# Performance work log

Hardware: AMD Instinct MI355X
Metric: run time of the kernel (lower is better)

Reference implementation:

```python
import jax, jax.numpy as jnp
import numpy as np

P = 16           # patch size
D = 768          # embed / feature dim (= 3*P*P)
T = 8            # number of task vectors
H_META = 192     # MetaNet hidden (= D // 4)


def patchify(x):
    # x: [B, 3, H, W] -> [B, N, 3*P*P]
    B, C, H, W = x.shape
    x = x.reshape(B, C, H // P, P, W // P, P)
    x = x.transpose(0, 2, 4, 1, 3, 5)
    return x.reshape(B, (H // P) * (W // P), C * P * P)


def encode(W1, b1, W2, b2, x):
    # base functional encoder f(params, x): shared weights over the batch
    patches = patchify(x)                       # [B, N, D]
    h = jax.nn.relu(patches @ W1 + b1)          # [B, N, D]
    pooled = h.mean(axis=1)                     # [B, D]
    return pooled @ W2 + b2                     # [B, D]


def setup_inputs() -> dict:
    key = jax.random.key(0)
    ks = jax.random.split(key, 14)
    B = 64
    s = 0.02
    return {
        "x":   jax.random.normal(ks[0], (B, 3, 224, 224), jnp.float32),
        # base model params
        "W1":  jax.random.normal(ks[1], (D, D), jnp.float32) * s,
        "b1":  jax.random.normal(ks[2], (D,), jnp.float32) * s,
        "W2":  jax.random.normal(ks[3], (D, D), jnp.float32) * s,
        "b2":  jax.random.normal(ks[4], (D,), jnp.float32) * s,
        # task-vector deltas (stacked over T tasks)
        "dW1": jax.random.normal(ks[5], (T, D, D), jnp.float32) * s,
        "db1": jax.random.normal(ks[6], (T, D), jnp.float32) * s,
        "dW2": jax.random.normal(ks[7], (T, D, D), jnp.float32) * s,
        "db2": jax.random.normal(ks[8], (T, D), jnp.float32) * s,
        # MetaNet (Linear-ReLU-Linear); zero-init in the original, random here
        "mw1": jax.random.normal(ks[9], (D, H_META), jnp.float32) * s,
        "mb1": jax.random.normal(ks[10], (H_META,), jnp.float32) * s,
        "mw2": jax.random.normal(ks[11], (H_META, T), jnp.float32) * s,
        "mb2": jax.random.normal(ks[12], (T,), jnp.float32) * s,
    }


def reference(x, W1, b1, W2, b2, dW1, db1, dW2, db2, mw1, mb1, mw2, mb2):
    # 1) base features with frozen base model (torch.no_grad)
    base = jax.lax.stop_gradient(encode(W1, b1, W2, b2, x))       # [B, D]
    # 2) per-sample mixing coefficients via MetaNet
    coefs = jax.nn.relu(base @ mw1 + mb1) @ mw2 + mb2             # [B, T]
    # 3) per-sample mixed parameters: p + sum_t c[b,t] * dp[t]
    nW1 = W1 + jnp.einsum("bt,tij->bij", coefs, dW1)              # [B, D, D]
    nb1 = b1 + coefs @ db1                                        # [B, D]
    nW2 = W2 + jnp.einsum("bt,tij->bij", coefs, dW2)              # [B, D, D]
    nb2 = b2 + coefs @ db2                                        # [B, D]
    # 4) batched per-sample forward with the mixed weights
    patches = patchify(x)                                         # [B, N, D]
    h = jax.nn.relu(jnp.einsum("bnd,bde->bne", patches, nW1) + nb1[:, None, :])
    pooled = h.mean(axis=1)                                       # [B, D]
    out = jnp.einsum("bd,bde->be", pooled, nW2) + nb2             # [B, D]
    return out
```

## Files before the change

kernel.cpp:

```cpp
#include <hip/hip_runtime.h>
#include <hip/hip_bf16.h>


typedef __bf16 bf16x8 __attribute__((ext_vector_type(8)));
typedef float f32x4 __attribute__((ext_vector_type(4)));
typedef __hip_bfloat16 bf16;

struct alignas(16) BF8 { bf16 h[8]; };

constexpr int BATCH = 64;
constexpr int NP    = 196;
constexpr int NPAD  = 256;
constexpr int DIM   = 768;
constexpr int NT    = 8;
constexpr size_t MSZ = (size_t)DIM * DIM;

__device__ __forceinline__ void async_cp16(const void* g, void* l) {
  __builtin_amdgcn_global_load_lds(
      (const __attribute__((address_space(1))) uint32_t*)g,
      (__attribute__((address_space(3))) uint32_t*)l, 16, 0, 0);
}

__global__ void k_patchify(const float* __restrict__ x, bf16* __restrict__ A) {
  int idx  = blockIdx.x * blockDim.x + threadIdx.x;
  int col4 = idx % (DIM / 4);
  int row  = idx / (DIM / 4);
  int d = col4 * 4;
  int b = row >> 8;
  int n = row & 255;
  bf16 tmp[4];
  if (n < NP) {
    int hp = n / 14, wp = n % 14;
    int c  = d >> 8;
    int rr = d & 255;
    int i = rr >> 4, j = rr & 15;
    const float* src = x + ((((size_t)b * 3 + c) * 224 + hp * 16 + i) * 224 + wp * 16 + j);
    float4 f = *(const float4*)src;
    tmp[0] = __float2bfloat16(f.x);
    tmp[1] = __float2bfloat16(f.y);
    tmp[2] = __float2bfloat16(f.z);
    tmp[3] = __float2bfloat16(f.w);
  } else {
    tmp[0] = tmp[1] = tmp[2] = tmp[3] = __float2bfloat16(0.0f);
  }
  *(ushort4*)(A + (size_t)row * DIM + d) = *(ushort4*)tmp;
}

__global__ void k_transpose_cast(const float* __restrict__ W1, const float* __restrict__ dW1,
                                 const float* __restrict__ W2, const float* __restrict__ dW2,
                                 bf16* __restrict__ WT) {
  __shared__ float tile[32][33];
  int mat = blockIdx.z;
  const float* src;
  if      (mat == 0) src = W1;
  else if (mat <= 8) src = dW1 + (size_t)(mat - 1) * MSZ;
  else if (mat == 9) src = W2;
  else               src = dW2 + (size_t)(mat - 10) * MSZ;
  int n0 = blockIdx.x * 32;
  int k0 = blockIdx.y * 32;
  int tx = threadIdx.x & 31, ty = threadIdx.x >> 5;
#pragma unroll
  for (int r = ty; r < 32; r += 8)
    tile[r][tx] = src[(size_t)(k0 + r) * DIM + n0 + tx];
  __syncthreads();
  bf16* dst = WT + (size_t)mat * MSZ;
#pragma unroll
  for (int r = ty; r < 32; r += 8)
    dst[(size_t)(n0 + r) * DIM + k0 + tx] = __float2bfloat16(tile[tx][r]);
}


template<int MIX>
__global__ __launch_bounds__(256, MIX ? 3 : 4)
void k_gemm_pool(const bf16* __restrict__ A,
                 const bf16* __restrict__ WT,
                 const float* __restrict__ b1,
                 const float* __restrict__ db1,
                 const float* __restrict__ coefs,
                 float* __restrict__ pooled) {
  __shared__ uint4 AslU[2][896];
  __shared__ uint4 BslU[2][256];

  int b  = blockIdx.x;
  int n0 = blockIdx.y * 64;
  int tid = threadIdx.x;
  int wave = tid >> 6, lane = tid & 63;
  int quad = lane >> 4, l16 = lane & 15;

  float cr[NT];
  if (MIX) {
#pragma unroll
    for (int t = 0; t < NT; t++) cr[t] = coefs[b * NT + t];
  }

  const bf16* Ag = A + (size_t)b * NPAD * DIM;
  f32x4 acc[4][4] = {};

  int gbase = (wave < 2) ? wave * 256 : 512 + (wave - 2) * 192;
  int gcnt  = (wave < 2) ? 4 : 3;
  auto stage_a = [&](int buf, int kt) {
    const bf16* Ak = Ag + kt * 32;
#pragma unroll
    for (int i = 0; i < 4; i++) {
      if (i < gcnt) {
        int s = gbase + i * 64 + lane;
        int r = s >> 2, c = (s & 3) ^ ((r ^ (r >> 2)) & 3);
        async_cp16(Ak + (size_t)r * DIM + c * 8, (void*)&AslU[buf][gbase + i * 64]);
      }
    }
  };
  auto stage_b_async = [&](int buf, int kt) {
    const bf16* Wk = WT + kt * 32;
    int s = tid;
    int r = s >> 2, c = (s & 3) ^ ((r ^ (r >> 2)) & 3);
    async_cp16(Wk + (size_t)(n0 + r) * DIM + c * 8, (void*)&BslU[buf][wave * 64]);
  };
  BF8 wreg[9];
  auto mixb_load = [&](int kt) {
    const bf16* Wk = WT + kt * 32;
    int s = tid;
    int r = s >> 2, c = (s & 3) ^ ((r ^ (r >> 2)) & 3);
    const bf16* p0 = Wk + (size_t)(n0 + r) * DIM + c * 8;
    wreg[0] = *(const BF8*)p0;
#pragma unroll
    for (int t = 0; t < NT; t++)
      wreg[1 + t] = *(const BF8*)(p0 + (size_t)(1 + t) * MSZ);
  };
  auto mixb_write = [&](int buf) {
    float m[8];
#pragma unroll
    for (int j = 0; j < 8; j++) m[j] = __bfloat162float(wreg[0].h[j]);
#pragma unroll
    for (int t = 0; t < NT; t++) {
      float cc = cr[t];
#pragma unroll
      for (int j = 0; j < 8; j++) m[j] += cc * __bfloat162float(wreg[1 + t].h[j]);
    }
    BF8 o;
#pragma unroll
    for (int j = 0; j < 8; j++) o.h[j] = __float2bfloat16(m[j]);
    BslU[buf][tid] = *(uint4*)&o;
  };

  stage_a(0, 0);
  if (MIX) { mixb_load(0); mixb_write(0); }
  else     stage_b_async(0, 0);
  __syncthreads();

  int cur = 0;
  for (int kt = 0; kt < 24; kt++) {
    if (kt < 23) {
      stage_a(cur ^ 1, kt + 1);
      if (MIX) mixb_load(kt + 1);
      else     stage_b_async(cur ^ 1, kt + 1);
    }
    const bf16* As = (const bf16*)AslU[cur];
    const bf16* Bs = (const bf16*)BslU[cur];
    bf16x8 bfr[4];
#pragma unroll
    for (int nf = 0; nf < 4; nf++) {
      int brow = nf * 16 + l16;
      int sc = quad ^ ((brow ^ (brow >> 2)) & 3);
      bfr[nf] = *(const bf16x8*)(Bs + ((size_t)brow * 4 + sc) * 8);
    }
#pragma unroll
    for (int mf = 0; mf < 4; mf++) {
      if (wave * 64 + mf * 16 < 224) {
        int arow = wave * 64 + mf * 16 + l16;
        int sc = quad ^ ((arow ^ (arow >> 2)) & 3);
        bf16x8 af = *(const bf16x8*)(As + ((size_t)arow * 4 + sc) * 8);
#pragma unroll
        for (int nf = 0; nf < 4; nf++)
          acc[mf][nf] = __builtin_amdgcn_mfma_f32_16x16x32_bf16(af, bfr[nf], acc[mf][nf], 0, 0, 0);
      }
    }
    if (MIX && kt < 23) mixb_write(cur ^ 1);
    __syncthreads();
    cur ^= 1;
  }

  float* red = (float*)&BslU[0][0];
  int m0 = wave * 64;
  float colsum[4];
#pragma unroll
  for (int nf = 0; nf < 4; nf++) {
    int col = n0 + nf * 16 + l16;
    float bias = b1[col];
    if (MIX) {
#pragma unroll
      for (int t = 0; t < NT; t++) bias += cr[t] * db1[t * DIM + col];
    }
    float s = 0.0f;
#pragma unroll
    for (int mf = 0; mf < 4; mf++) {
      int rbase = m0 + mf * 16 + quad * 4;
#pragma unroll
      for (int r = 0; r < 4; r++) {
        if (rbase + r < NP) s += fmaxf(acc[mf][nf][r] + bias, 0.0f);
      }
    }
    s += __shfl_xor(s, 16, 64);
    s += __shfl_xor(s, 32, 64);
    colsum[nf] = s;
  }
  if (lane < 16) {
#pragma unroll
    for (int nf = 0; nf < 4; nf++) red[wave * 64 + nf * 16 + lane] = colsum[nf];
  }
  __syncthreads();
  if (tid < 64) {
    float s = red[tid] + red[64 + tid] + red[128 + tid] + red[192 + tid];
    pooled[(size_t)b * DIM + n0 + tid] = s * (1.0f / 196.0f);
  }
}

__global__ __launch_bounds__(256, 2)
void k_gemm2(const float* __restrict__ Af,
             const bf16* __restrict__ WT,
             int matbase,
             const float* __restrict__ bias,
             float* __restrict__ Y) {
  __shared__ uint4 AslU[64 * 8];
  __shared__ uint4 BslU[64 * 8];
  int n0  = blockIdx.x * 64;
  int mat = blockIdx.y;
  int tid = threadIdx.x, wave = tid >> 6, lane = tid & 63;
  int quad = lane >> 4, l16 = lane & 15;
  f32x4 acc[4] = {};
  const bf16* Wm = WT + (size_t)(matbase + mat) * MSZ;
  for (int k0 = 0; k0 < DIM; k0 += 64) {
#pragma unroll
    for (int i = 0; i < 2; i++) {
      int g = tid + i * 256;
      int r = g >> 3, c = g & 7;
      const float* src = Af + (size_t)r * DIM + k0 + c * 8;
      float4 xa = ((const float4*)src)[0];
      float4 xb = ((const float4*)src)[1];
      BF8 o;
      o.h[0] = __float2bfloat16(xa.x); o.h[1] = __float2bfloat16(xa.y);
      o.h[2] = __float2bfloat16(xa.z); o.h[3] = __float2bfloat16(xa.w);
      o.h[4] = __float2bfloat16(xb.x); o.h[5] = __float2bfloat16(xb.y);
      o.h[6] = __float2bfloat16(xb.z); o.h[7] = __float2bfloat16(xb.w);
      AslU[r * 8 + (c ^ (r & 7))] = *(uint4*)&o;
      BslU[r * 8 + (c ^ (r & 7))] = *(const uint4*)(Wm + (size_t)(n0 + r) * DIM + k0 + c * 8);
    }
    __syncthreads();
    const bf16* As = (const bf16*)AslU;
    const bf16* Bs = (const bf16*)BslU;
#pragma unroll
    for (int ks = 0; ks < 2; ks++) {
      int brow = wave * 16 + l16;
      bf16x8 bfr = *(const bf16x8*)(Bs + (size_t)(brow * 8 + ((ks * 4 + quad) ^ (brow & 7))) * 8);
#pragma unroll
      for (int mf = 0; mf < 4; mf++) {
        int arow = mf * 16 + l16;
        bf16x8 af = *(const bf16x8*)(As + (size_t)(arow * 8 + ((ks * 4 + quad) ^ (arow & 7))) * 8);
        acc[mf] = __builtin_amdgcn_mfma_f32_16x16x32_bf16(af, bfr, acc[mf], 0, 0, 0);
      }
    }
    __syncthreads();
  }
#pragma unroll
  for (int mf = 0; mf < 4; mf++) {
#pragma unroll
    for (int r = 0; r < 4; r++) {
      int row = mf * 16 + quad * 4 + r;
      int col = n0 + wave * 16 + l16;
      float v = acc[mf][r];
      if (bias) v += bias[col];
      Y[((size_t)mat * 64 + row) * DIM + col] = v;
    }
  }
}

__global__ void k_metanet(const float* __restrict__ base,
                          const float* __restrict__ mw1, const float* __restrict__ mb1,
                          const float* __restrict__ mw2, const float* __restrict__ mb2,
                          float* __restrict__ coefs) {
  __shared__ float bl[DIM];
  __shared__ float hl[192];
  int b = blockIdx.x, tid = threadIdx.x;
  for (int i = tid; i < DIM; i += 192) bl[i] = base[(size_t)b * DIM + i];
  __syncthreads();
  float s = mb1[tid];
  for (int k = 0; k < DIM; k++) s += bl[k] * mw1[(size_t)k * 192 + tid];
  hl[tid] = fmaxf(s, 0.0f);
  __syncthreads();
  if (tid < NT) {
    float c = mb2[tid];
    for (int j = 0; j < 192; j++) c += hl[j] * mw2[(size_t)j * NT + tid];
    coefs[b * NT + tid] = c;
  }
}

__global__ void k_combine(const float* __restrict__ Y,
                          const float* __restrict__ coefs,
                          const float* __restrict__ b2,
                          const float* __restrict__ db2,
                          float* __restrict__ out) {
  int idx = blockIdx.x * 256 + threadIdx.x;
  int b = idx / DIM, e = idx % DIM;
  float v = Y[(size_t)b * DIM + e] + b2[e];
#pragma unroll
  for (int t = 0; t < NT; t++) {
    float c = coefs[b * NT + t];
    v += c * (Y[((size_t)(1 + t) * 64 + b) * DIM + e] + db2[(size_t)t * DIM + e]);
  }
  out[idx] = v;
}

extern "C" void kernel_launch(void* const* d_in, const int* in_sizes, int n_in,
                              void* d_out, int out_size, void* d_ws, size_t ws_size,
                              hipStream_t stream) {
  const float* x   = (const float*)d_in[0];
  const float* W1  = (const float*)d_in[1];
  const float* b1  = (const float*)d_in[2];
  const float* W2  = (const float*)d_in[3];
  const float* b2  = (const float*)d_in[4];
  const float* dW1 = (const float*)d_in[5];
  const float* db1 = (const float*)d_in[6];
  const float* dW2 = (const float*)d_in[7];
  const float* db2 = (const float*)d_in[8];
  const float* mw1 = (const float*)d_in[9];
  const float* mb1 = (const float*)d_in[10];
  const float* mw2 = (const float*)d_in[11];
  const float* mb2 = (const float*)d_in[12];
  float* out = (float*)d_out;
  (void)in_sizes; (void)n_in; (void)out_size; (void)ws_size;

  char* ws = (char*)d_ws;
  bf16*  A_bf    = (bf16*) (ws);
  bf16*  WT      = (bf16*) (ws + 25165824);
  float* pooledA = (float*)(ws + 46399488);
  float* pooledB = (float*)(ws + 46596096);
  float* coefs   = (float*)(ws + 46792704);
  float* base    = (float*)(ws + 46794752);
  float* Y       = (float*)(ws + 46991360);

  k_patchify<<<dim3((BATCH * NPAD * (DIM / 4)) / 256), 256, 0, stream>>>(x, A_bf);
  k_transpose_cast<<<dim3(24, 24, 18), 256, 0, stream>>>(W1, dW1, W2, dW2, WT);
  k_gemm_pool<0><<<dim3(BATCH, DIM / 64), 256, 0, stream>>>(A_bf, WT, b1, db1, nullptr, pooledA);
  k_gemm2<<<dim3(DIM / 64, 1), 256, 0, stream>>>(pooledA, WT, 9, b2, base);
  k_metanet<<<dim3(BATCH), 192, 0, stream>>>(base, mw1, mb1, mw2, mb2, coefs);
  k_gemm_pool<1><<<dim3(BATCH, DIM / 64), 256, 0, stream>>>(A_bf, WT, b1, db1, coefs, pooledB);
  k_gemm2<<<dim3(DIM / 64, 9), 256, 0, stream>>>(pooledB, WT, 9, nullptr, Y);
  k_combine<<<dim3((BATCH * DIM) / 256), 256, 0, stream>>>(Y, coefs, b2, db2, out);
}
```

Before: 301.7 us.

## Triple-buffer A tiles with manual vmcnt waits and new LDS swizzle

The GEMM-pool kernel now keeps three A-tile LDS buffers, prefetching two k-steps ahead with async global-to-LDS copies. Each iteration uses a single barrier plus explicit s_waitcnt vmcnt counts in place of two __syncthreads. The non-mix path loads B through registers instead of async LDS copies, and the LDS swizzle changes to an 8-slot XOR over row pairs to reduce bank conflicts. This costs more LDS per block, and the non-mix variant's occupancy target drops from 4 to 3. Correctness depends on the hand-tuned wait counts matching the number of outstanding loads per wave.

```diff
diff --git a/kernel.cpp b/kernel.cpp
--- a/kernel.cpp
+++ b/kernel.cpp
@@ -70,15 +70,17 @@
 }
 
 
+#define WAITVM(N) asm volatile("s_waitcnt vmcnt(" #N ")" ::: "memory")
+
 template<int MIX>
-__global__ __launch_bounds__(256, MIX ? 3 : 4)
+__global__ __launch_bounds__(256, 3)
 void k_gemm_pool(const bf16* __restrict__ A,
                  const bf16* __restrict__ WT,
                  const float* __restrict__ b1,
                  const float* __restrict__ db1,
                  const float* __restrict__ coefs,
                  float* __restrict__ pooled) {
-  __shared__ uint4 AslU[2][896];
+  __shared__ uint4 AslU[3][896];
   __shared__ uint4 BslU[2][256];
 
   int b  = blockIdx.x;
@@ -104,79 +106,97 @@
     for (int i = 0; i < 4; i++) {
       if (i < gcnt) {
         int s = gbase + i * 64 + lane;
-        int r = s >> 2, c = (s & 3) ^ ((r ^ (r >> 2)) & 3);
+        int p = s >> 3, u = (s & 7) ^ (p & 7);
+        int r = 2 * p + (u >> 2), c = u & 3;
         async_cp16(Ak + (size_t)r * DIM + c * 8, (void*)&AslU[buf][gbase + i * 64]);
       }
     }
   };
-  auto stage_b_async = [&](int buf, int kt) {
-    const bf16* Wk = WT + kt * 32;
-    int s = tid;
-    int r = s >> 2, c = (s & 3) ^ ((r ^ (r >> 2)) & 3);
-    async_cp16(Wk + (size_t)(n0 + r) * DIM + c * 8, (void*)&BslU[buf][wave * 64]);
+
+  int bp = tid >> 3, bu = (tid & 7) ^ (bp & 7);
+  int brow_st = 2 * bp + (bu >> 2), bcol_st = bu & 3;
+  const bf16* Wrow = WT + (size_t)(n0 + brow_st) * DIM + bcol_st * 8;
+
+  BF8 wreg[MIX ? 9 : 1];
+  auto breg_load = [&](int kt) {
+    const bf16* p0 = Wrow + kt * 32;
+    wreg[0] = *(const BF8*)p0;
+    if (MIX) {
+#pragma unroll
+      for (int t = 0; t < NT; t++)
+        wreg[1 + t] = *(const BF8*)(p0 + (size_t)(1 + t) * MSZ);
+    }
   };
-  BF8 wreg[9];
-  auto mixb_load = [&](int kt) {
-    const bf16* Wk = WT + kt * 32;
-    int s = tid;
-    int r = s >> 2, c = (s & 3) ^ ((r ^ (r >> 2)) & 3);
-    const bf16* p0 = Wk + (size_t)(n0 + r) * DIM + c * 8;
-    wreg[0] = *(const BF8*)p0;
-#pragma unroll
-    for (int t = 0; t < NT; t++)
-      wreg[1 + t] = *(const BF8*)(p0 + (size_t)(1 + t) * MSZ);
+  auto breg_write = [&](int buf) {
+    if (MIX) {
+      float m[8];
+#pragma unroll
+      for (int j = 0; j < 8; j++) m[j] = __bfloat162float(wreg[0].h[j]);
+#pragma unroll
+      for (int t = 0; t < NT; t++) {
+        float cc = cr[t];
+#pragma unroll
+        for (int j = 0; j < 8; j++) m[j] += cc * __bfloat162float(wreg[1 + t].h[j]);
+      }
+      BF8 o;
+#pragma unroll
+      for (int j = 0; j < 8; j++) o.h[j] = __float2bfloat16(m[j]);
+      BslU[buf][tid] = *(uint4*)&o;
+    } else {
+      BslU[buf][tid] = *(uint4*)&wreg[0];
+    }
   };
-  auto mixb_write = [&](int buf) {
-    float m[8];
-#pragma unroll
-    for (int j = 0; j < 8; j++) m[j] = __bfloat162float(wreg[0].h[j]);
-#pragma unroll
-    for (int t = 0; t < NT; t++) {
-      float cc = cr[t];
-#pragma unroll
-      for (int j = 0; j < 8; j++) m[j] += cc * __bfloat162float(wreg[1 + t].h[j]);
-    }
-    BF8 o;
-#pragma unroll
-    for (int j = 0; j < 8; j++) o.h[j] = __float2bfloat16(m[j]);
-    BslU[buf][tid] = *(uint4*)&o;
+
+  auto gslot = [&](int row, int kq) {
+    return (size_t)((row >> 1) * 8 + ((4 * (row & 1) + kq) ^ ((row >> 1) & 7)));
   };
 
   stage_a(0, 0);
-  if (MIX) { mixb_load(0); mixb_write(0); }
-  else     stage_b_async(0, 0);
-  __syncthreads();
-
-  int cur = 0;
+  stage_a(1, 1);
+  breg_load(0);
+  WAITVM(0);
+  __builtin_amdgcn_sched_barrier(0);
+  breg_write(0);
+  asm volatile("s_waitcnt lgkmcnt(0)" ::: "memory");
+
+  int bufA = 0, stgA = 2, bufB = 0;
   for (int kt = 0; kt < 24; kt++) {
-    if (kt < 23) {
-      stage_a(cur ^ 1, kt + 1);
-      if (MIX) mixb_load(kt + 1);
-      else     stage_b_async(cur ^ 1, kt + 1);
-    }
-    const bf16* As = (const bf16*)AslU[cur];
-    const bf16* Bs = (const bf16*)BslU[cur];
+    __builtin_amdgcn_s_barrier();
+    if (kt < 23) breg_load(kt + 1);
+    __builtin_amdgcn_sched_barrier(0);
+    if (kt < 22) stage_a(stgA, kt + 2);
+    __builtin_amdgcn_sched_barrier(0);
+    const bf16* As = (const bf16*)AslU[bufA];
+    const bf16* Bs = (const bf16*)BslU[bufB];
     bf16x8 bfr[4];
 #pragma unroll
     for (int nf = 0; nf < 4; nf++) {
       int brow = nf * 16 + l16;
-      int sc = quad ^ ((brow ^ (brow >> 2)) & 3);
-      bfr[nf] = *(const bf16x8*)(Bs + ((size_t)brow * 4 + sc) * 8);
+      bfr[nf] = *(const bf16x8*)(Bs + gslot(brow, quad) * 8);
     }
 #pragma unroll
     for (int mf = 0; mf < 4; mf++) {
       if (wave * 64 + mf * 16 < 224) {
         int arow = wave * 64 + mf * 16 + l16;
-        int sc = quad ^ ((arow ^ (arow >> 2)) & 3);
-        bf16x8 af = *(const bf16x8*)(As + ((size_t)arow * 4 + sc) * 8);
+        bf16x8 af = *(const bf16x8*)(As + gslot(arow, quad) * 8);
 #pragma unroll
         for (int nf = 0; nf < 4; nf++)
           acc[mf][nf] = __builtin_amdgcn_mfma_f32_16x16x32_bf16(af, bfr[nf], acc[mf][nf], 0, 0, 0);
       }
     }
-    if (MIX && kt < 23) mixb_write(cur ^ 1);
-    __syncthreads();
-    cur ^= 1;
+    if (kt < 22) {
+      if (wave < 2) WAITVM(4); else WAITVM(3);
+    } else if (kt < 23) {
+      WAITVM(0);
+    }
+    __builtin_amdgcn_sched_barrier(0);
+    if (kt < 23) {
+      breg_write(bufB ^ 1);
+      asm volatile("s_waitcnt lgkmcnt(0)" ::: "memory");
+    }
+    bufA = (bufA == 2) ? 0 : bufA + 1;
+    stgA = (stgA == 2) ? 0 : stgA + 1;
+    bufB ^= 1;
   }
 
   float* red = (float*)&BslU[0][0];
```

New measurement: 297.4 us. No clear change (-1.4%).
